# Kernel tuning notes

Hardware: AMD Instinct MI355X
Metric: run time of the kernel (lower is better)

Reference implementation:

```python
import jax, jax.numpy as jnp
import numpy as np

B, P, Q, D = 16, 4096, 1024, 256


def setup_inputs() -> dict:
    key = jax.random.key(0)
    k1, k2, k3, k4 = jax.random.split(key, 4)
    return {
        "passage_encodes": jax.random.normal(k1, (B, P, D), dtype=jnp.float32),
        "question_encodes": jax.random.normal(k2, (B, Q, D), dtype=jnp.float32),
        "w_attn": jax.random.normal(k3, (2 * D, 1), dtype=jnp.float32) * (1.0 / np.sqrt(2 * D)),
        "b_attn": jnp.zeros((1,), dtype=jnp.float32),
        "w_out": jax.random.normal(k4, (2 * D, 256), dtype=jnp.float32) * (1.0 / np.sqrt(2 * D)),
        "b_out": jnp.zeros((256,), dtype=jnp.float32),
    }


def reference(passage_encodes, question_encodes, w_attn, b_attn, w_out, b_out):
    # similarity matrix [B, P, Q]
    sim = jnp.einsum('bpd,bqd->bpq', passage_encodes, question_encodes)
    # context-to-question attention
    c2q = jax.nn.softmax(sim, axis=-1)                       # [B, P, Q]
    ctx2q = jnp.einsum('bpq,bqd->bpd', c2q, question_encodes)  # [B, P, D]
    # question-to-context attention (softmax over row-max)
    q2c = jax.nn.softmax(jnp.max(sim, axis=-1), axis=-1)     # [B, P]
    q2c_vec = jnp.einsum('bp,bpd->bd', q2c, passage_encodes)  # [B, D]
    tp = jnp.tanh(passage_encodes)
    concat = jnp.concatenate([
        tp * jnp.tanh(ctx2q),
        tp * jnp.tanh(q2c_vec)[:, None, :],  # broadcast instead of repeat
    ], axis=-1)                                              # [B, P, 2D]
    # attention reducer: linear -> softmax over sequence -> weighted sum
    w = jax.nn.softmax(jnp.einsum('bpc,co->bp', concat, w_attn) + b_attn[0], axis=1)
    reduced = jnp.einsum('bp,bpc->bc', w, concat)            # [B, 2D]
    return reduced @ w_out + b_out                            # [B, output_dim]
```

## Files before the change

kernel.cpp:

```cpp
#include <hip/hip_runtime.h>
#include <cmath>

#define BB 16
#define PP 4096
#define QQ 1024
#define DD 256

typedef __attribute__((ext_vector_type(8))) short short8;
typedef __attribute__((ext_vector_type(4))) float floatx4;
typedef __attribute__((ext_vector_type(4))) _Float16 half4;
typedef __attribute__((ext_vector_type(4))) unsigned short ushort4v;

static __device__ inline ushort bf16_rne(float x) {
  unsigned u = __float_as_uint(x);
  unsigned r = (u + 0x7fffu + ((u >> 16) & 1u)) >> 16;
  return (ushort)r;
}
static __device__ inline float bf16f(ushort h) { return __uint_as_float(((unsigned)h) << 16); }

static __device__ inline float ftanh(float x) {
  float e = __expf(2.0f * x);
  return 1.0f - 2.0f * __builtin_amdgcn_rcpf(e + 1.0f);
}

static __device__ inline void gl16(const void* g, void* l) {
  __builtin_amdgcn_global_load_lds(
      (const __attribute__((address_space(1))) unsigned int*)g,
      (__attribute__((address_space(3))) unsigned int*)l, 16, 0, 0);
}

__global__ __launch_bounds__(256) void kQprep(
    const float* __restrict__ ques, ushort* __restrict__ qb)
{
  const int b = blockIdx.y, qt = blockIdx.x;
  __shared__ float tile[32][260];
  const int tid = threadIdx.x;
  const float* src = ques + ((size_t)b * QQ + qt * 32) * DD;
  for (int i = tid; i < 32 * 64; i += 256) {
    int r = i >> 6, c = (i & 63) << 2;
    *(float4*)&tile[r][c] = *(const float4*)(src + r * DD + c);
  }
  __syncthreads();
  ushort* blob = qb + (size_t)(b * 32 + qt) * 24576;
  {
    int r = tid >> 3;
    int j0 = (tid & 7) * 4;
#pragma unroll
    for (int jj = 0; jj < 4; ++jj) {
      int j = j0 + jj;
      ushort h8[8], l8[8];
#pragma unroll
      for (int e = 0; e < 8; ++e) {
        float x = tile[r][j * 8 + e];
        ushort h = bf16_rne(x);
        h8[e] = h; l8[e] = bf16_rne(x - bf16f(h));
      }
      int g = r * 32 + (j ^ (r & 7));
      *(uint4*)&blob[(size_t)g * 8] = *(uint4*)h8;
      *(uint4*)&blob[8192 + (size_t)g * 8] = *(uint4*)l8;
    }
  }
  {
    int d = tid;
    int s = (d >> 1) & 3;
    ushort h32[32];
#pragma unroll
    for (int r = 0; r < 32; ++r) h32[r] = bf16_rne(tile[r][d]);
#pragma unroll
    for (int k = 0; k < 4; ++k)
      *(uint4*)&blob[16384 + (size_t)d * 32 + (k ^ s) * 8] = *(uint4*)&h32[k * 8];
  }
}

__global__ __launch_bounds__(512, 2) void kA(
    const float* __restrict__ pass, const ushort* __restrict__ qb,
    const float* __restrict__ w_attn,
    _Float16* __restrict__ first_h, _Float16* __restrict__ tp_h,
    float* __restrict__ rowmax, float* __restrict__ logit1)
{
  __shared__ alignas(16) char sm[135168];

  const int b    = blockIdx.y;
  const int p0   = blockIdx.x * 128;
  const int tid  = threadIdx.x;
  const int w    = tid >> 6;
  const int lane = tid & 63;
  const int l15  = lane & 15;
  const int quad = lane >> 4;
  const int swz  = l15 & 7;

  const int qt1  = w >> 2;
  const int pt1  = (w & 3) * 2;
  const int dgrp = w >> 1;
  const int phs  = (w & 1) * 4;

  short8 bhi[2][8], blo[2][8];
#pragma unroll
  for (int pt = 0; pt < 2; ++pt) {
    const float* prow = pass + (((size_t)b * PP + p0 + (pt1 + pt) * 16 + l15) * DD);
#pragma unroll
    for (int c = 0; c < 8; ++c) {
      const float* p8 = prow + c * 32 + quad * 8;
      float4 x0 = *(const float4*)p8;
      float4 x1 = *(const float4*)(p8 + 4);
      float xs[8] = {x0.x, x0.y, x0.z, x0.w, x1.x, x1.y, x1.z, x1.w};
#pragma unroll
      for (int j = 0; j < 8; ++j) {
        ushort h  = bf16_rne(xs[j]);
        ushort lo = bf16_rne(xs[j] - bf16f(h));
        bhi[pt][c][j] = (short)h;
        blo[pt][c][j] = (short)lo;
      }
    }
  }

  const int gb    = (qt1 * 16 + l15) * 256;
  const int vtoff = l15 * 32 + ((quad ^ ((l15 >> 1) & 3)) * 8);

  ushort* PbufH = (ushort*)(sm + 98304);
  ushort* PbufL = (ushort*)(sm + 106496);
  const int pgd  = qt1 * 2 + (quad >> 1);
  const int psub = (quad & 1) * 4;

  const ushort* tb = qb + (size_t)b * 32 * 24576;
  const int dma_l = w * 3072 + lane * 8;
  const int dma_s = w * 6144 + lane * 16;

  floatx4 accO[4][4];
#pragma unroll
  for (int i = 0; i < 4; ++i)
#pragma unroll
    for (int k = 0; k < 4; ++k) accO[i][k] = (floatx4){0.f, 0.f, 0.f, 0.f};
  float ps0 = 0.f, ps1 = 0.f, mx0 = -INFINITY, mx1 = -INFINITY;

  {
    const ushort* gs = tb + dma_l;
    char* ld = sm + dma_s;
#pragma unroll
    for (int i = 0; i < 6; ++i) gl16(gs + i * 512, ld + i * 1024);
  }
  __syncthreads();

  for (int t = 0; t < 32; ++t) {
    const char* cur = sm + (t & 1) * 49152;
    if (t < 31) {
      const ushort* gs = tb + (size_t)(t + 1) * 24576 + dma_l;
      char* ld = sm + ((t + 1) & 1) * 49152 + dma_s;
#pragma unroll
      for (int i = 0; i < 6; ++i) gl16(gs + i * 512, ld + i * 1024);
    }

    const ushort* Qhi = (const ushort*)cur;
    const ushort* Qlo = (const ushort*)(cur + 16384);
    floatx4 s0 = (floatx4){0.f, 0.f, 0.f, 0.f};
    floatx4 s1 = (floatx4){0.f, 0.f, 0.f, 0.f};
    __builtin_amdgcn_s_setprio(1);
#pragma unroll
    for (int c = 0; c < 8; ++c) {
      const int go = gb + (((4 * c + quad) ^ swz) << 3);
      short8 ah = *(const short8*)&Qhi[go];
      short8 al = *(const short8*)&Qlo[go];
      s0 = __builtin_amdgcn_mfma_f32_16x16x32_bf16(ah, bhi[0][c], s0, 0, 0, 0);
      s0 = __builtin_amdgcn_mfma_f32_16x16x32_bf16(ah, blo[0][c], s0, 0, 0, 0);
      s0 = __builtin_amdgcn_mfma_f32_16x16x32_bf16(al, bhi[0][c], s0, 0, 0, 0);
      s1 = __builtin_amdgcn_mfma_f32_16x16x32_bf16(ah, bhi[1][c], s1, 0, 0, 0);
      s1 = __builtin_amdgcn_mfma_f32_16x16x32_bf16(ah, blo[1][c], s1, 0, 0, 0);
      s1 = __builtin_amdgcn_mfma_f32_16x16x32_bf16(al, bhi[1][c], s1, 0, 0, 0);
    }
    __builtin_amdgcn_s_setprio(0);

    {
      ushort4v ph, pl;
#pragma unroll
      for (int r = 0; r < 4; ++r) {
        float s = s0[r];
        mx0 = fmaxf(mx0, s);
        float x = __expf(s - 60.f);
        ps0 += x;
        ushort h = bf16_rne(x);
        ph[r] = h;
        pl[r] = bf16_rne(x - bf16f(h));
      }
      const int wi = ((pt1 * 16 + l15) * 4 + (pgd ^ (l15 & 3))) * 8 + psub;
      *(ushort4v*)&PbufH[wi] = ph;
      *(ushort4v*)&PbufL[wi] = pl;
    }
    {
      ushort4v ph, pl;
#pragma unroll
      for (int r = 0; r < 4; ++r) {
        float s = s1[r];
        mx1 = fmaxf(mx1, s);
        float x = __expf(s - 60.f);
        ps1 += x;
        ushort h = bf16_rne(x);
        ph[r] = h;
        pl[r] = bf16_rne(x - bf16f(h));
      }
      const int wi = (((pt1 + 1) * 16 + l15) * 4 + (pgd ^ (l15 & 3))) * 8 + psub;
      *(ushort4v*)&PbufH[wi] = ph;
      *(ushort4v*)&PbufL[wi] = pl;
    }

    asm volatile("s_waitcnt lgkmcnt(0)" ::: "memory");
    __builtin_amdgcn_s_barrier();
    __builtin_amdgcn_sched_barrier(0);

    const ushort* TQ = (const ushort*)(cur + 32768);
    short8 vhi[4];
#pragma unroll
    for (int k = 0; k < 4; ++k)
      vhi[k] = *(const short8*)&TQ[(dgrp * 4 + k) * 512 + vtoff];
    __builtin_amdgcn_s_setprio(1);
#pragma unroll
    for (int pt = 0; pt < 4; ++pt) {
      const int ri = (((phs + pt) * 16 + l15) * 4 + (quad ^ (l15 & 3))) * 8;
      short8 phh = *(const short8*)&PbufH[ri];
      short8 pll = *(const short8*)&PbufL[ri];
#pragma unroll
      for (int k = 0; k < 4; ++k) {
        accO[pt][k] = __builtin_amdgcn_mfma_f32_16x16x32_bf16(phh, vhi[k], accO[pt][k], 0, 0, 0);
        accO[pt][k] = __builtin_amdgcn_mfma_f32_16x16x32_bf16(pll, vhi[k], accO[pt][k], 0, 0, 0);
      }
    }
    __builtin_amdgcn_s_setprio(0);
    __syncthreads();
  }

  ps0 += __shfl_xor(ps0, 16); ps0 += __shfl_xor(ps0, 32);
  ps1 += __shfl_xor(ps1, 16); ps1 += __shfl_xor(ps1, 32);
  mx0 = fmaxf(mx0, __shfl_xor(mx0, 16)); mx0 = fmaxf(mx0, __shfl_xor(mx0, 32));
  mx1 = fmaxf(mx1, __shfl_xor(mx1, 16)); mx1 = fmaxf(mx1, __shfl_xor(mx1, 32));

  float* psb = (float*)(sm + 133120);
  float* mxb = (float*)(sm + 134144);
  if (lane < 16) {
    psb[(qt1 * 8 + pt1) * 16 + l15]     = ps0;
    psb[(qt1 * 8 + pt1 + 1) * 16 + l15] = ps1;
    mxb[(qt1 * 8 + pt1) * 16 + l15]     = mx0;
    mxb[(qt1 * 8 + pt1 + 1) * 16 + l15] = mx1;
  }
  __syncthreads();
  const float pstot = psb[w * 16 + l15] + psb[128 + w * 16 + l15];
  const float mxtot = fmaxf(mxb[w * 16 + l15], mxb[128 + w * 16 + l15]);
  const size_t rowoff = (size_t)b * PP + p0 + w * 16;
  if (lane < 16) rowmax[rowoff + lane] = mxtot;

  float* Of = (float*)sm;
#pragma unroll
  for (int pt = 0; pt < 4; ++pt)
#pragma unroll
    for (int k = 0; k < 4; ++k)
#pragma unroll
      for (int r = 0; r < 4; ++r)
        Of[((w & 1) * 64 + pt * 16 + quad * 4 + r) * 260 + dgrp * 64 + k * 16 + l15] =
            accO[pt][k][r];
  __syncthreads();

  const float4 w1 = *(const float4*)(w_attn + lane * 4);
#pragma unroll
  for (int j = 0; j < 16; ++j) {
    float4 o = *(const float4*)&Of[(w * 16 + j) * 260 + lane * 4];
    float linv = 1.f / __shfl(pstot, j);
    float4 pv4 = *(const float4*)(pass + (rowoff + j) * DD + lane * 4);
    float tpx = ftanh(pv4.x), tpy = ftanh(pv4.y), tpz = ftanh(pv4.z), tpw = ftanh(pv4.w);
    float4 f;
    f.x = tpx * ftanh(o.x * linv);
    f.y = tpy * ftanh(o.y * linv);
    f.z = tpz * ftanh(o.z * linv);
    f.w = tpw * ftanh(o.w * linv);
    half4 fh = {(_Float16)f.x, (_Float16)f.y, (_Float16)f.z, (_Float16)f.w};
    half4 th = {(_Float16)tpx, (_Float16)tpy, (_Float16)tpz, (_Float16)tpw};
    *(half4*)(first_h + (rowoff + j) * DD + lane * 4) = fh;
    *(half4*)(tp_h + (rowoff + j) * DD + lane * 4) = th;
    float part = f.x * w1.x + f.y * w1.y + f.z * w1.z + f.w * w1.w;
    part += __shfl_xor(part, 1);  part += __shfl_xor(part, 2);
    part += __shfl_xor(part, 4);  part += __shfl_xor(part, 8);
    part += __shfl_xor(part, 16); part += __shfl_xor(part, 32);
    if (lane == 0) logit1[rowoff + j] = part;
  }
}

__global__ __launch_bounds__(256) void kB2(
    const float* __restrict__ pass, const float* __restrict__ rowmax,
    float* __restrict__ numpart, float* __restrict__ denpart)
{
  const int b = blockIdx.y, chunk = blockIdx.x;
  const int tid = threadIdx.x, r = tid >> 6, ln = tid & 63;
  __shared__ float sacc[4][64][4];
  __shared__ float sden[4][64];
  const float* rm = rowmax + (size_t)b * PP + chunk * 128;
  const float* pb = pass + ((size_t)b * PP + chunk * 128) * DD;
  float4 acc = make_float4(0.f, 0.f, 0.f, 0.f);
  float den = 0.f;
  for (int p = r; p < 128; p += 4) {
    float wgt = __expf(rm[p] - 60.f);
    float4 v = *(const float4*)(pb + (size_t)p * DD + ln * 4);
    acc.x += wgt * v.x; acc.y += wgt * v.y;
    acc.z += wgt * v.z; acc.w += wgt * v.w;
    den += wgt;
  }
  *(float4*)&sacc[r][ln][0] = acc;
  sden[r][ln] = den;
  __syncthreads();
  if (r == 0) {
    float4 s;
    s.x = sacc[0][ln][0] + sacc[1][ln][0] + sacc[2][ln][0] + sacc[3][ln][0];
    s.y = sacc[0][ln][1] + sacc[1][ln][1] + sacc[2][ln][1] + sacc[3][ln][1];
    s.z = sacc[0][ln][2] + sacc[1][ln][2] + sacc[2][ln][2] + sacc[3][ln][2];
    s.w = sacc[0][ln][3] + sacc[1][ln][3] + sacc[2][ln][3] + sacc[3][ln][3];
    *(float4*)(numpart + (size_t)(chunk * 16 + b) * DD + ln * 4) = s;
    if (ln == 0)
      denpart[chunk * 16 + b] = sden[0][0] + sden[1][0] + sden[2][0] + sden[3][0];
  }
}

__global__ void kB3(const float* __restrict__ numpart, const float* __restrict__ denpart,
                    const float* __restrict__ w_attn,
                    float* __restrict__ tq, float* __restrict__ w2tq)
{
  const int b = blockIdx.x, d = threadIdx.x;
  float den = 0.f, num = 0.f;
#pragma unroll
  for (int c = 0; c < 32; ++c) {
    den += denpart[c * 16 + b];
    num += numpart[(size_t)(c * 16 + b) * DD + d];
  }
  float t = ftanh(num / den);
  tq[b * DD + d] = t;
  w2tq[b * DD + d] = w_attn[DD + d] * t;
}

__global__ __launch_bounds__(256) void kC(
    const _Float16* __restrict__ tp_h, const float* __restrict__ logit1,
    const float* __restrict__ w2tq, float* __restrict__ el)
{
  const int b = blockIdx.y, chunk = blockIdx.x;
  const int wave = threadIdx.x >> 6, lane = threadIdx.x & 63;
  const float4 wv = *(const float4*)(w2tq + b * DD + (lane << 2));
  const int pbase = chunk * 128 + wave * 32;
  for (int j = 0; j < 32; ++j) {
    int p = pbase + j;
    half4 tv = *(const half4*)(tp_h + ((size_t)b * PP + p) * DD + (lane << 2));
    float part = (float)tv.x * wv.x + (float)tv.y * wv.y +
                 (float)tv.z * wv.z + (float)tv.w * wv.w;
    part += __shfl_xor(part, 1);  part += __shfl_xor(part, 2);
    part += __shfl_xor(part, 4);  part += __shfl_xor(part, 8);
    part += __shfl_xor(part, 16); part += __shfl_xor(part, 32);
    if (lane == 0)
      el[(size_t)b * PP + p] = __expf(logit1[(size_t)b * PP + p] + part);
  }
}

__global__ __launch_bounds__(256) void kE(
    const _Float16* __restrict__ tp_h, const _Float16* __restrict__ first_h,
    const float* __restrict__ el,
    float* __restrict__ r1part, float* __restrict__ r2part, float* __restrict__ den2part)
{
  const int b = blockIdx.y, chunk = blockIdx.x;
  const int tid = threadIdx.x, r = tid >> 6, ln = tid & 63;
  __shared__ float s1[4][64][4];
  __shared__ float s2[4][64][4];
  __shared__ float sd[4][64];
  const float* ev = el + (size_t)b * PP + chunk * 128;
  const size_t base = ((size_t)b * PP + chunk * 128) * DD;
  float a1[4] = {0.f, 0.f, 0.f, 0.f}, a2[4] = {0.f, 0.f, 0.f, 0.f};
  float den = 0.f;
  for (int p = r; p < 128; p += 4) {
    float wgt = ev[p];
    half4 f = *(const half4*)(first_h + base + (size_t)p * DD + ln * 4);
    half4 t = *(const half4*)(tp_h + base + (size_t)p * DD + ln * 4);
    a1[0] += wgt * (float)f.x; a1[1] += wgt * (float)f.y;
    a1[2] += wgt * (float)f.z; a1[3] += wgt * (float)f.w;
    a2[0] += wgt * (float)t.x; a2[1] += wgt * (float)t.y;
    a2[2] += wgt * (float)t.z; a2[3] += wgt * (float)t.w;
    den += wgt;
  }
  *(float4*)&s1[r][ln][0] = *(float4*)a1;
  *(float4*)&s2[r][ln][0] = *(float4*)a2;
  sd[r][ln] = den;
  __syncthreads();
  if (r == 0) {
    float o1[4], o2[4];
#pragma unroll
    for (int i = 0; i < 4; ++i) {
      o1[i] = s1[0][ln][i] + s1[1][ln][i] + s1[2][ln][i] + s1[3][ln][i];
      o2[i] = s2[0][ln][i] + s2[1][ln][i] + s2[2][ln][i] + s2[3][ln][i];
    }
    *(float4*)(r1part + (size_t)(chunk * 16 + b) * DD + ln * 4) = *(float4*)o1;
    *(float4*)(r2part + (size_t)(chunk * 16 + b) * DD + ln * 4) = *(float4*)o2;
    if (ln == 0)
      den2part[chunk * 16 + b] = sd[0][0] + sd[1][0] + sd[2][0] + sd[3][0];
  }
}

__global__ __launch_bounds__(256) void kF(
    const float* __restrict__ r1part, const float* __restrict__ r2part,
    const float* __restrict__ den2part, const float* __restrict__ tq,
    const float* __restrict__ w_out, const float* __restrict__ b_out,
    float* __restrict__ out)
{
  const int b = blockIdx.x, o = threadIdx.x;
  __shared__ float R1[256], R2[256];
  float den = 0.f, red1 = 0.f, red2 = 0.f;
#pragma unroll
  for (int c = 0; c < 32; ++c) {
    den += den2part[c * 16 + b];
    red1 += r1part[(size_t)(c * 16 + b) * DD + o];
    red2 += r2part[(size_t)(c * 16 + b) * DD + o];
  }
  float inv = 1.f / den;
  R1[o] = red1 * inv;
  R2[o] = red2 * inv * tq[b * DD + o];
  __syncthreads();
  float acc = b_out[o];
  for (int k = 0; k < DD; ++k)
    acc += R1[k] * w_out[k * 256 + o];
  for (int k = 0; k < DD; ++k)
    acc += R2[k] * w_out[(DD + k) * 256 + o];
  out[b * 256 + o] = acc;
}

extern "C" void kernel_launch(void* const* d_in, const int* in_sizes, int n_in,
                              void* d_out, int out_size, void* d_ws, size_t ws_size,
                              hipStream_t stream) {
  const float* pass   = (const float*)d_in[0];
  const float* ques   = (const float*)d_in[1];
  const float* w_attn = (const float*)d_in[2];
  const float* w_out  = (const float*)d_in[4];
  const float* b_out  = (const float*)d_in[5];
  float* out = (float*)d_out;

  float* ws       = (float*)d_ws;
  float* rowmax   = ws;
  float* logit1   = rowmax   + (size_t)BB * PP;
  float* el       = logit1   + (size_t)BB * PP;
  float* numpart  = el       + (size_t)BB * PP;
  float* denpart  = numpart  + (size_t)32 * BB * DD;
  float* r1part   = denpart  + 32 * BB;
  float* r2part   = r1part   + (size_t)32 * BB * DD;
  float* den2part = r2part   + (size_t)32 * BB * DD;
  float* tq       = den2part + 32 * BB;
  float* w2tq     = tq       + BB * DD;
  ushort* qbb     = (ushort*)(w2tq + BB * DD);
  _Float16* first_h = (_Float16*)(qbb + (size_t)BB * 32 * 24576);
  _Float16* tp_h    = first_h + (size_t)BB * PP * DD;

  kQprep<<<dim3(QQ / 32, BB), 256, 0, stream>>>(ques, qbb);
  kA    <<<dim3(PP / 128, BB), 512, 0, stream>>>(pass, qbb, w_attn,
                                                 first_h, tp_h, rowmax, logit1);
  kB2   <<<dim3(32, BB), 256, 0, stream>>>(pass, rowmax, numpart, denpart);
  kB3   <<<BB, 256, 0, stream>>>(numpart, denpart, w_attn, tq, w2tq);
  kC    <<<dim3(32, BB), 256, 0, stream>>>(tp_h, logit1, w2tq, el);
  kE    <<<dim3(32, BB), 256, 0, stream>>>(tp_h, first_h, el, r1part, r2part, den2part);
  kF    <<<BB, 256, 0, stream>>>(r1part, r2part, den2part, tq, w_out, b_out, out);
}
```

Before: 381.1 us.

## Split QK^T reduction dimension across wave pairs to halve passage register fragments

Each wave now holds only half of the D dimension of its passage rows in bf16 hi/lo registers and computes partial scores for both 16-row question subtiles. Partial sums are exchanged with the partner wave through a new shared-memory buffer before the exp/softmax stage. This halves the persistent B-fragment register footprint, likely to relieve register pressure at two blocks per CU. The cost is an extra LDS round trip and an extra barrier per Q tile.

```diff
diff --git a/kernel.cpp b/kernel.cpp
--- a/kernel.cpp
+++ b/kernel.cpp
@@ -89,18 +89,16 @@
   const int quad = lane >> 4;
   const int swz  = l15 & 7;
 
-  const int qt1  = w >> 2;
-  const int pt1  = (w & 3) * 2;
-  const int dgrp = w >> 1;
-  const int phs  = (w & 1) * 4;
-
-  short8 bhi[2][8], blo[2][8];
+  const int pp = w >> 1;
+  const int kh = w & 1;
+
+  short8 bhi[2][4], blo[2][4];
 #pragma unroll
   for (int pt = 0; pt < 2; ++pt) {
-    const float* prow = pass + (((size_t)b * PP + p0 + (pt1 + pt) * 16 + l15) * DD);
-#pragma unroll
-    for (int c = 0; c < 8; ++c) {
-      const float* p8 = prow + c * 32 + quad * 8;
+    const float* prow = pass + (((size_t)b * PP + p0 + pp * 32 + pt * 16 + l15) * DD);
+#pragma unroll
+    for (int c = 0; c < 4; ++c) {
+      const float* p8 = prow + (kh * 4 + c) * 32 + quad * 8;
       float4 x0 = *(const float4*)p8;
       float4 x1 = *(const float4*)(p8 + 4);
       float xs[8] = {x0.x, x0.y, x0.z, x0.w, x1.x, x1.y, x1.z, x1.w};
@@ -114,13 +112,12 @@
     }
   }
 
-  const int gb    = (qt1 * 16 + l15) * 256;
-  const int vtoff = l15 * 32 + ((quad ^ ((l15 >> 1) & 3)) * 8);
-
   ushort* PbufH = (ushort*)(sm + 98304);
   ushort* PbufL = (ushort*)(sm + 106496);
-  const int pgd  = qt1 * 2 + (quad >> 1);
-  const int psub = (quad & 1) * 4;
+  float*  Sbuf  = (float*)(sm + 114688);
+  const int pgd   = kh * 2 + (quad >> 1);
+  const int psub  = (quad & 1) * 4;
+  const int vtoff = l15 * 32 + ((quad ^ ((l15 >> 1) & 3)) * 8);
 
   const ushort* tb = qb + (size_t)b * 32 * 24576;
   const int dma_l = w * 3072 + lane * 8;
@@ -152,69 +149,98 @@
 
     const ushort* Qhi = (const ushort*)cur;
     const ushort* Qlo = (const ushort*)(cur + 16384);
-    floatx4 s0 = (floatx4){0.f, 0.f, 0.f, 0.f};
-    floatx4 s1 = (floatx4){0.f, 0.f, 0.f, 0.f};
+    floatx4 s00 = (floatx4){0.f, 0.f, 0.f, 0.f};
+    floatx4 s01 = (floatx4){0.f, 0.f, 0.f, 0.f};
+    floatx4 s10 = (floatx4){0.f, 0.f, 0.f, 0.f};
+    floatx4 s11 = (floatx4){0.f, 0.f, 0.f, 0.f};
     __builtin_amdgcn_s_setprio(1);
 #pragma unroll
-    for (int c = 0; c < 8; ++c) {
-      const int go = gb + (((4 * c + quad) ^ swz) << 3);
-      short8 ah = *(const short8*)&Qhi[go];
-      short8 al = *(const short8*)&Qlo[go];
-      s0 = __builtin_amdgcn_mfma_f32_16x16x32_bf16(ah, bhi[0][c], s0, 0, 0, 0);
-      s0 = __builtin_amdgcn_mfma_f32_16x16x32_bf16(ah, blo[0][c], s0, 0, 0, 0);
-      s0 = __builtin_amdgcn_mfma_f32_16x16x32_bf16(al, bhi[0][c], s0, 0, 0, 0);
-      s1 = __builtin_amdgcn_mfma_f32_16x16x32_bf16(ah, bhi[1][c], s1, 0, 0, 0);
-      s1 = __builtin_amdgcn_mfma_f32_16x16x32_bf16(ah, blo[1][c], s1, 0, 0, 0);
-      s1 = __builtin_amdgcn_mfma_f32_16x16x32_bf16(al, bhi[1][c], s1, 0, 0, 0);
+    for (int c = 0; c < 4; ++c) {
+      const int go0 = l15 * 256 + (((kh * 16 + c * 4 + quad) ^ swz) << 3);
+      short8 a0h = *(const short8*)&Qhi[go0];
+      short8 a0l = *(const short8*)&Qlo[go0];
+      short8 a1h = *(const short8*)&Qhi[go0 + 4096];
+      short8 a1l = *(const short8*)&Qlo[go0 + 4096];
+      s00 = __builtin_amdgcn_mfma_f32_16x16x32_bf16(a0h, bhi[0][c], s00, 0, 0, 0);
+      s00 = __builtin_amdgcn_mfma_f32_16x16x32_bf16(a0h, blo[0][c], s00, 0, 0, 0);
+      s00 = __builtin_amdgcn_mfma_f32_16x16x32_bf16(a0l, bhi[0][c], s00, 0, 0, 0);
+      s01 = __builtin_amdgcn_mfma_f32_16x16x32_bf16(a0h, bhi[1][c], s01, 0, 0, 0);
+      s01 = __builtin_amdgcn_mfma_f32_16x16x32_bf16(a0h, blo[1][c], s01, 0, 0, 0);
+      s01 = __builtin_amdgcn_mfma_f32_16x16x32_bf16(a0l, bhi[1][c], s01, 0, 0, 0);
+      s10 = __builtin_amdgcn_mfma_f32_16x16x32_bf16(a1h, bhi[0][c], s10, 0, 0, 0);
+      s10 = __builtin_amdgcn_mfma_f32_16x16x32_bf16(a1h, blo[0][c], s10, 0, 0, 0);
+      s10 = __builtin_amdgcn_mfma_f32_16x16x32_bf16(a1l, bhi[0][c], s10, 0, 0, 0);
+      s11 = __builtin_amdgcn_mfma_f32_16x16x32_bf16(a1h, bhi[1][c], s11, 0, 0, 0);
+      s11 = __builtin_amdgcn_mfma_f32_16x16x32_bf16(a1h, blo[1][c], s11, 0, 0, 0);
+      s11 = __builtin_amdgcn_mfma_f32_16x16x32_bf16(a1l, bhi[1][c], s11, 0, 0, 0);
     }
     __builtin_amdgcn_s_setprio(0);
 
     {
-      ushort4v ph, pl;
-#pragma unroll
-      for (int r = 0; r < 4; ++r) {
-        float s = s0[r];
-        mx0 = fmaxf(mx0, s);
-        float x = __expf(s - 60.f);
-        ps0 += x;
-        ushort h = bf16_rne(x);
-        ph[r] = h;
-        pl[r] = bf16_rne(x - bf16f(h));
-      }
-      const int wi = ((pt1 * 16 + l15) * 4 + (pgd ^ (l15 & 3))) * 8 + psub;
-      *(ushort4v*)&PbufH[wi] = ph;
-      *(ushort4v*)&PbufL[wi] = pl;
-    }
-    {
-      ushort4v ph, pl;
-#pragma unroll
-      for (int r = 0; r < 4; ++r) {
-        float s = s1[r];
-        mx1 = fmaxf(mx1, s);
-        float x = __expf(s - 60.f);
-        ps1 += x;
-        ushort h = bf16_rne(x);
-        ph[r] = h;
-        pl[r] = bf16_rne(x - bf16f(h));
-      }
-      const int wi = (((pt1 + 1) * 16 + l15) * 4 + (pgd ^ (l15 & 3))) * 8 + psub;
-      *(ushort4v*)&PbufH[wi] = ph;
-      *(ushort4v*)&PbufL[wi] = pl;
-    }
-
+      float* dst = Sbuf + pp * 1024 + (1 - kh) * 512 + lane * 4;
+      floatx4 w0 = kh ? s00 : s10;
+      floatx4 w1 = kh ? s01 : s11;
+      *(floatx4*)dst = w0;
+      *(floatx4*)(dst + 256) = w1;
+    }
     asm volatile("s_waitcnt lgkmcnt(0)" ::: "memory");
     __builtin_amdgcn_s_barrier();
     __builtin_amdgcn_sched_barrier(0);
+    floatx4 sA, sB;
+    {
+      const float* src = Sbuf + pp * 1024 + kh * 512 + lane * 4;
+      floatx4 o0 = *(const floatx4*)src;
+      floatx4 o1 = *(const floatx4*)(src + 256);
+      floatx4 own0 = kh ? s10 : s00;
+      floatx4 own1 = kh ? s11 : s01;
+      sA = own0 + o0;
+      sB = own1 + o1;
+    }
+
+    {
+      ushort4v ph, pl;
+#pragma unroll
+      for (int r = 0; r < 4; ++r) {
+        float v = sA[r];
+        mx0 = fmaxf(mx0, v);
+        float x = __expf(v - 60.f);
+        ps0 += x;
+        ushort h = bf16_rne(x);
+        ph[r] = h; pl[r] = bf16_rne(x - bf16f(h));
+      }
+      const int wi = (((pp * 2 + 0) * 16 + l15) * 4 + (pgd ^ (l15 & 3))) * 8 + psub;
+      *(ushort4v*)&PbufH[wi] = ph;
+      *(ushort4v*)&PbufL[wi] = pl;
+    }
+    {
+      ushort4v ph, pl;
+#pragma unroll
+      for (int r = 0; r < 4; ++r) {
+        float v = sB[r];
+        mx1 = fmaxf(mx1, v);
+        float x = __expf(v - 60.f);
+        ps1 += x;
+        ushort h = bf16_rne(x);
+        ph[r] = h; pl[r] = bf16_rne(x - bf16f(h));
+      }
+      const int wi = (((pp * 2 + 1) * 16 + l15) * 4 + (pgd ^ (l15 & 3))) * 8 + psub;
+      *(ushort4v*)&PbufH[wi] = ph;
+      *(ushort4v*)&PbufL[wi] = pl;
+    }
+
+    asm volatile("s_waitcnt lgkmcnt(0)" ::: "memory");
+    __builtin_amdgcn_s_barrier();
+    __builtin_amdgcn_sched_barrier(0);
 
     const ushort* TQ = (const ushort*)(cur + 32768);
     short8 vhi[4];
 #pragma unroll
     for (int k = 0; k < 4; ++k)
-      vhi[k] = *(const short8*)&TQ[(dgrp * 4 + k) * 512 + vtoff];
+      vhi[k] = *(const short8*)&TQ[(pp * 4 + k) * 512 + vtoff];
     __builtin_amdgcn_s_setprio(1);
 #pragma unroll
     for (int pt = 0; pt < 4; ++pt) {
-      const int ri = (((phs + pt) * 16 + l15) * 4 + (quad ^ (l15 & 3))) * 8;
+      const int ri = (((kh * 4 + pt) * 16 + l15) * 4 + (quad ^ (l15 & 3))) * 8;
       short8 phh = *(const short8*)&PbufH[ri];
       short8 pll = *(const short8*)&PbufL[ri];
 #pragma unroll
@@ -235,10 +261,10 @@
   float* psb = (float*)(sm + 133120);
   float* mxb = (float*)(sm + 134144);
   if (lane < 16) {
-    psb[(qt1 * 8 + pt1) * 16 + l15]     = ps0;
-    psb[(qt1 * 8 + pt1 + 1) * 16 + l15] = ps1;
-    mxb[(qt1 * 8 + pt1) * 16 + l15]     = mx0;
-    mxb[(qt1 * 8 + pt1 + 1) * 16 + l15] = mx1;
+    psb[kh * 128 + pp * 32 + l15]      = ps0;
+    psb[kh * 128 + pp * 32 + 16 + l15] = ps1;
+    mxb[kh * 128 + pp * 32 + l15]      = mx0;
+    mxb[kh * 128 + pp * 32 + 16 + l15] = mx1;
   }
   __syncthreads();
   const float pstot = psb[w * 16 + l15] + psb[128 + w * 16 + l15];
@@ -253,7 +279,7 @@
     for (int k = 0; k < 4; ++k)
 #pragma unroll
       for (int r = 0; r < 4; ++r)
-        Of[((w & 1) * 64 + pt * 16 + quad * 4 + r) * 260 + dgrp * 64 + k * 16 + l15] =
+        Of[(kh * 64 + pt * 16 + quad * 4 + r) * 260 + pp * 64 + k * 16 + l15] =
             accO[pt][k][r];
   __syncthreads();
 
```

Result: faster. 362.1 us (-5.0%).
